# Performance work log

Measured on AMD Instinct MI355X. Metric: run time of the kernel, lower is better.

## Reference

```python
import jax, jax.numpy as jnp
import numpy as np

K = 256           # number of selected features (init kwarg k)
NUM_SAMPLES = 8   # init kwarg num_samples
BATCH = 256
NUM_FEATURES = 20000


def setup_inputs() -> dict:
    key = jax.random.key(0)
    logits = jax.random.normal(key, (BATCH, NUM_FEATURES, 1), dtype=jnp.float32)
    return {"logits": logits, "tau": 1, "training": 0}


def reference(logits, tau, training):
    # Eval branch of SubsetLayer.forward (training=False).
    # logits: [B, N, 1]
    B, N, _ = logits.shape
    scores = logits[..., 0]                       # [B, N]
    _, idx = jax.lax.top_k(scores, K)             # idx: [B, K]
    # k-hot mask built directly by scatter (equivalent to one_hot(...).sum(1))
    khot = jnp.zeros((B, N), dtype=jnp.float32)
    khot = khot.at[jnp.arange(B)[:, None], idx].set(1.0)  # [B, N]
    # unsqueeze(0).unsqueeze(-1).expand(num_samples, -1, -1, -1)
    out = jnp.broadcast_to(khot[None, :, :, None], (NUM_SAMPLES, B, N, 1))
    return out
```

## Files before the change

kernel.cpp:

```cpp
#include <hip/hip_runtime.h>

#define BATCH   256
#define NFEAT   20000
#define NVEC    (NFEAT / 4)
#define KSEL    256
#define NSAMP   8
#define CAP     2048

typedef unsigned long long u64;
typedef float __attribute__((ext_vector_type(4))) f32x4;

__device__ __forceinline__ unsigned fmap(float f) {
    unsigned u = __float_as_uint(f);
    return (u & 0x80000000u) ? ~u : (u | 0x80000000u);
}

__device__ __forceinline__ void select_bin_wave0(const unsigned* hist, int nbins, int w,
                                                 int* s_d, int* s_w, int lane) {
    for (int base = nbins - 1; base >= 0; base -= 64) {
        int bin = base - lane;
        unsigned c = (bin >= 0) ? hist[bin] : 0u;
        unsigned p = c;
#pragma unroll
        for (int off = 1; off < 64; off <<= 1) {
            unsigned t = __shfl_up(p, off);
            if (lane >= off) p += t;
        }
        unsigned long long m = __ballot(p >= (unsigned)w);
        if (m) {
            int l = __ffsll(m) - 1;
            if (lane == l) { *s_d = bin; *s_w = w - (int)(p - c); }
            return;
        }
        w -= (int)__shfl(p, 63);
    }
    if (lane == 0) { *s_d = 0; *s_w = 1; }
}

__device__ __forceinline__ void pick64(const unsigned* arr, int w, int lane,
                                       int* s_idx, int* s_w) {
    unsigned c = arr[63 - lane];
    unsigned p = c;
#pragma unroll
    for (int off = 1; off < 64; off <<= 1) {
        unsigned t = __shfl_up(p, off);
        if (lane >= off) p += t;
    }
    unsigned long long m = __ballot(p >= (unsigned)w);
    if (m) {
        int l = __ffsll(m) - 1;
        if (lane == l) { *s_idx = 63 - l; *s_w = w - (int)(p - c); }
    } else if (lane == 0) { *s_idx = 0; *s_w = 1; }
}

__global__ __launch_bounds__(1024) void topk_select(const float* __restrict__ logits,
                                                    u64* __restrict__ rowthr) {
    const int b = blockIdx.x, tid = threadIdx.x;
    const int lane = tid & 63, wave = tid >> 6;
    const float4* __restrict__ row4 = (const float4*)(logits + (size_t)b * NFEAT);

    __shared__ unsigned hist[4096];
    __shared__ u64 cand[CAP];
    __shared__ unsigned csum[64];
    __shared__ int s_d, s_w;
    __shared__ unsigned s_cnt;
    __shared__ u64 s_thr;
    __shared__ int s_run, s_cut, s_wc[16];

    float4 v[5];
#pragma unroll
    for (int j = 0; j < 5; ++j) {
        const int i4 = tid + j * 1024;
        v[j] = row4[(i4 < NVEC) ? i4 : (NVEC - 1)];
    }
#pragma unroll
    for (int j = 0; j < 4; ++j) hist[tid + j * 1024] = 0;
    __syncthreads();

    unsigned kk[5][4];
#pragma unroll
    for (int j = 0; j < 5; ++j) {
        kk[j][0] = fmap(v[j].x); kk[j][1] = fmap(v[j].y);
        kk[j][2] = fmap(v[j].z); kk[j][3] = fmap(v[j].w);
    }
#pragma unroll
    for (int j = 0; j < 4; ++j) {
#pragma unroll
        for (int e = 0; e < 4; ++e) atomicAdd(&hist[kk[j][e] >> 20], 1u);
    }
    if (tid + 4096 < NVEC) {
#pragma unroll
        for (int e = 0; e < 4; ++e) atomicAdd(&hist[kk[4][e] >> 20], 1u);
    }
    __syncthreads();

    unsigned keypref; int w;
    {
#pragma unroll
        for (int j = 0; j < 4; ++j) {
            const int c = wave * 4 + j;
            unsigned x = hist[c * 64 + lane];
#pragma unroll
            for (int off = 32; off; off >>= 1) x += __shfl_down(x, off);
            if (lane == 0) csum[c] = x;
        }
        __syncthreads();
        if (wave == 0) pick64(csum, KSEL, lane, &s_d, &s_w);
        __syncthreads();
        const int chunk = s_d; const int w0 = s_w;
        if (wave == 0) pick64(&hist[chunk * 64], w0, lane, &s_d, &s_w);
        if (tid == 0) s_cnt = 0;
        __syncthreads();
        keypref = (unsigned)(chunk * 64 + s_d);
        w = s_w;
    }
    int shift = 20;

    unsigned C;
    for (;;) {
#pragma unroll
        for (int j = 0; j < 5; ++j) {
            const int i4 = tid + j * 1024;
            if (i4 < NVEC) {
#pragma unroll
                for (int e = 0; e < 4; ++e) {
                    const unsigned k = kk[j][e];
                    if ((k >> shift) == keypref) {
                        unsigned p = atomicAdd(&s_cnt, 1u);
                        if (p < CAP) cand[p] = ((u64)k << 32) | (unsigned)~(4 * i4 + e);
                    }
                }
            }
        }
        __syncthreads();
        C = s_cnt;
        if (C <= CAP || shift == 0) break;

        const int nb = (shift >= 12) ? 12 : shift;
        const int nsh = shift - nb;
        for (int i = tid; i < (1 << nb); i += 1024) hist[i] = 0;
        __syncthreads();
#pragma unroll
        for (int j = 0; j < 5; ++j) {
            const int i4 = tid + j * 1024;
            if (i4 < NVEC) {
#pragma unroll
                for (int e = 0; e < 4; ++e) {
                    const unsigned k = kk[j][e];
                    if ((k >> shift) == keypref)
                        atomicAdd(&hist[(k >> nsh) & ((1u << nb) - 1u)], 1u);
                }
            }
        }
        __syncthreads();
        if (wave == 0) select_bin_wave0(hist, 1 << nb, w, &s_d, &s_w, lane);
        if (tid == 0) s_cnt = 0;
        __syncthreads();
        keypref = (keypref << nb) | (unsigned)s_d;
        w = s_w;
        shift = nsh;
    }

    if (C <= CAP) {
        for (int i = tid; i < (int)C; i += 1024) {
            const u64 ci = cand[i];
            int cgt = 0;
            for (int j = 0; j < (int)C; ++j) cgt += (cand[j] > ci) ? 1 : 0;
            if (cgt == w - 1) s_thr = ci;
        }
        __syncthreads();
    } else {
        if (tid == 0) { s_run = 0; s_cut = 0; }
        __syncthreads();
#pragma unroll 1
        for (int j = 0; j < 5; ++j) {
            const int i4 = tid + j * 1024;
            bool eq[4];
            int cnt4 = 0;
#pragma unroll
            for (int e = 0; e < 4; ++e) {
                eq[e] = (i4 < NVEC) && (kk[j][e] == keypref);
                cnt4 += eq[e] ? 1 : 0;
            }
            unsigned p = (unsigned)cnt4;
#pragma unroll
            for (int off = 1; off < 64; off <<= 1) {
                unsigned t = __shfl_up(p, off);
                if (lane >= off) p += t;
            }
            const unsigned excl = p - (unsigned)cnt4;
            if (lane == 63) s_wc[wave] = (int)p;
            __syncthreads();
            int off0 = s_run + (int)excl;
            for (int x = 0; x < wave; ++x) off0 += s_wc[x];
#pragma unroll
            for (int e = 0; e < 4; ++e) {
                if (eq[e]) { if (off0 == w - 1) s_cut = 4 * i4 + e; ++off0; }
            }
            __syncthreads();
            if (tid == 0) { int t = 0; for (int x = 0; x < 16; ++x) t += s_wc[x]; s_run += t; }
            __syncthreads();
            if (s_run >= w) break;
        }
        if (tid == 0) s_thr = ((u64)keypref << 32) | (unsigned)~s_cut;
        __syncthreads();
    }

    if (tid == 0) rowthr[b] = s_thr;
}

__global__ __launch_bounds__(256) void write_out(const float* __restrict__ logits,
                                                 const u64* __restrict__ rowthr,
                                                 float* __restrict__ out) {
    const int b = blockIdx.y;
    const int q = blockIdx.x * 256 + threadIdx.x;
    if (q >= NVEC) return;

    const u64 thr = rowthr[b];
    const unsigned thr_k = (unsigned)(thr >> 32);
    const unsigned thr_l = (unsigned)thr;
    const int n = q * 4;
    const float4 v = *reinterpret_cast<const float4*>(logits + (size_t)b * NFEAT + n);

    f32x4 m;
    {
        const float* vf = &v.x;
#pragma unroll
        for (int j = 0; j < 4; ++j) {
            const unsigned k = fmap(vf[j]);
            const bool sel = (k > thr_k) || (k == thr_k && (unsigned)~(n + j) >= thr_l);
            m[j] = sel ? 1.0f : 0.0f;
        }
    }

#pragma unroll
    for (int s = 0; s < NSAMP; ++s) {
        *reinterpret_cast<f32x4*>(out + ((size_t)s * BATCH + b) * NFEAT + n) = m;
    }
}

extern "C" void kernel_launch(void* const* d_in, const int* in_sizes, int n_in,
                              void* d_out, int out_size, void* d_ws, size_t ws_size,
                              hipStream_t stream) {
    const float* logits = (const float*)d_in[0];
    float* out = (float*)d_out;
    u64* rowthr = (u64*)d_ws;

    topk_select<<<BATCH, 1024, 0, stream>>>(logits, rowthr);

    dim3 grid((NVEC + 255) / 256, BATCH);
    write_out<<<grid, 256, 0, stream>>>(logits, rowthr, out);
}
```

Before: 41.38 us.

## Replace candidate-buffer rank sort with iterative 8-bit radix refinement until unique

The top-k threshold search no longer collects candidates into a shared buffer and ranks them with an O(C^2) pairwise count. It keeps refining the key prefix with 8-bit histogram passes, each using a two-level pick64 scan, until the selected bin holds a single element or all bits are resolved. This removes the quadratic candidate ranking and the 16KB candidate array from shared memory. In exchange it may need several more histogram passes and barriers per row.

```diff
diff --git a/kernel.cpp b/kernel.cpp
--- a/kernel.cpp
+++ b/kernel.cpp
@@ -5,7 +5,6 @@
 #define NVEC    (NFEAT / 4)
 #define KSEL    256
 #define NSAMP   8
-#define CAP     2048
 
 typedef unsigned long long u64;
 typedef float __attribute__((ext_vector_type(4))) f32x4;
@@ -13,28 +12,6 @@
 __device__ __forceinline__ unsigned fmap(float f) {
     unsigned u = __float_as_uint(f);
     return (u & 0x80000000u) ? ~u : (u | 0x80000000u);
-}
-
-__device__ __forceinline__ void select_bin_wave0(const unsigned* hist, int nbins, int w,
-                                                 int* s_d, int* s_w, int lane) {
-    for (int base = nbins - 1; base >= 0; base -= 64) {
-        int bin = base - lane;
-        unsigned c = (bin >= 0) ? hist[bin] : 0u;
-        unsigned p = c;
-#pragma unroll
-        for (int off = 1; off < 64; off <<= 1) {
-            unsigned t = __shfl_up(p, off);
-            if (lane >= off) p += t;
-        }
-        unsigned long long m = __ballot(p >= (unsigned)w);
-        if (m) {
-            int l = __ffsll(m) - 1;
-            if (lane == l) { *s_d = bin; *s_w = w - (int)(p - c); }
-            return;
-        }
-        w -= (int)__shfl(p, 63);
-    }
-    if (lane == 0) { *s_d = 0; *s_w = 1; }
 }
 
 __device__ __forceinline__ void pick64(const unsigned* arr, int w, int lane,
@@ -60,10 +37,8 @@
     const float4* __restrict__ row4 = (const float4*)(logits + (size_t)b * NFEAT);
 
     __shared__ unsigned hist[4096];
-    __shared__ u64 cand[CAP];
     __shared__ unsigned csum[64];
     __shared__ int s_d, s_w;
-    __shared__ unsigned s_cnt;
     __shared__ u64 s_thr;
     __shared__ int s_run, s_cut, s_wc[16];
 
@@ -94,30 +69,38 @@
     }
     __syncthreads();
 
-    unsigned keypref; int w;
+    unsigned P; int w;
     {
 #pragma unroll
         for (int j = 0; j < 4; ++j) {
-            const int c = wave * 4 + j;
-            unsigned x = hist[c * 64 + lane];
+            const int cc = wave * 4 + j;
+            unsigned x = hist[cc * 64 + lane];
 #pragma unroll
             for (int off = 32; off; off >>= 1) x += __shfl_down(x, off);
-            if (lane == 0) csum[c] = x;
+            if (lane == 0) csum[cc] = x;
         }
         __syncthreads();
         if (wave == 0) pick64(csum, KSEL, lane, &s_d, &s_w);
         __syncthreads();
         const int chunk = s_d; const int w0 = s_w;
         if (wave == 0) pick64(&hist[chunk * 64], w0, lane, &s_d, &s_w);
-        if (tid == 0) s_cnt = 0;
-        __syncthreads();
-        keypref = (unsigned)(chunk * 64 + s_d);
+        __syncthreads();
+        P = (unsigned)(chunk * 64 + s_d);
         w = s_w;
     }
+    unsigned cnt = hist[P];
     int shift = 20;
 
-    unsigned C;
-    for (;;) {
+    while (cnt > 1u && shift > 0) {
+        const int nb  = (shift >= 8) ? 8 : shift;
+        const int nsh = shift - nb;
+        const int NB  = 1 << nb;
+        const int nz  = (NB > 64) ? NB : 64;
+        __syncthreads();
+        if (tid < nz) hist[tid] = 0;
+        if (tid >= 4 && tid < 64) csum[tid] = 0;
+        __syncthreads();
+
 #pragma unroll
         for (int j = 0; j < 5; ++j) {
             const int i4 = tid + j * 1024;
@@ -125,21 +108,40 @@
 #pragma unroll
                 for (int e = 0; e < 4; ++e) {
                     const unsigned k = kk[j][e];
-                    if ((k >> shift) == keypref) {
-                        unsigned p = atomicAdd(&s_cnt, 1u);
-                        if (p < CAP) cand[p] = ((u64)k << 32) | (unsigned)~(4 * i4 + e);
-                    }
+                    if ((k >> shift) == P)
+                        atomicAdd(&hist[(k >> nsh) & (unsigned)(NB - 1)], 1u);
                 }
             }
         }
         __syncthreads();
-        C = s_cnt;
-        if (C <= CAP || shift == 0) break;
-
-        const int nb = (shift >= 12) ? 12 : shift;
-        const int nsh = shift - nb;
-        for (int i = tid; i < (1 << nb); i += 1024) hist[i] = 0;
-        __syncthreads();
+
+        unsigned d;
+        if (NB > 64) {
+            if (wave < 4) {
+                unsigned x = hist[wave * 64 + lane];
+#pragma unroll
+                for (int off = 32; off; off >>= 1) x += __shfl_down(x, off);
+                if (lane == 0) csum[wave] = x;
+            }
+            __syncthreads();
+            if (wave == 0) pick64(csum, w, lane, &s_d, &s_w);
+            __syncthreads();
+            const int chunk2 = s_d; const int w1 = s_w;
+            if (wave == 0) pick64(&hist[chunk2 * 64], w1, lane, &s_d, &s_w);
+            __syncthreads();
+            d = (unsigned)(chunk2 * 64 + s_d);
+        } else {
+            if (wave == 0) pick64(hist, w, lane, &s_d, &s_w);
+            __syncthreads();
+            d = (unsigned)s_d;
+        }
+        w = s_w;
+        cnt = hist[d];
+        P = (P << nb) | d;
+        shift = nsh;
+    }
+
+    if (cnt == 1u) {
 #pragma unroll
         for (int j = 0; j < 5; ++j) {
             const int i4 = tid + j * 1024;
@@ -147,26 +149,10 @@
 #pragma unroll
                 for (int e = 0; e < 4; ++e) {
                     const unsigned k = kk[j][e];
-                    if ((k >> shift) == keypref)
-                        atomicAdd(&hist[(k >> nsh) & ((1u << nb) - 1u)], 1u);
+                    if ((k >> shift) == P)
+                        s_thr = ((u64)k << 32) | (unsigned)~(4 * i4 + e);
                 }
             }
-        }
-        __syncthreads();
-        if (wave == 0) select_bin_wave0(hist, 1 << nb, w, &s_d, &s_w, lane);
-        if (tid == 0) s_cnt = 0;
-        __syncthreads();
-        keypref = (keypref << nb) | (unsigned)s_d;
-        w = s_w;
-        shift = nsh;
-    }
-
-    if (C <= CAP) {
-        for (int i = tid; i < (int)C; i += 1024) {
-            const u64 ci = cand[i];
-            int cgt = 0;
-            for (int j = 0; j < (int)C; ++j) cgt += (cand[j] > ci) ? 1 : 0;
-            if (cgt == w - 1) s_thr = ci;
         }
         __syncthreads();
     } else {
@@ -179,7 +165,7 @@
             int cnt4 = 0;
 #pragma unroll
             for (int e = 0; e < 4; ++e) {
-                eq[e] = (i4 < NVEC) && (kk[j][e] == keypref);
+                eq[e] = (i4 < NVEC) && (kk[j][e] == P);
                 cnt4 += eq[e] ? 1 : 0;
             }
             unsigned p = (unsigned)cnt4;
@@ -202,7 +188,7 @@
             __syncthreads();
             if (s_run >= w) break;
         }
-        if (tid == 0) s_thr = ((u64)keypref << 32) | (unsigned)~s_cut;
+        if (tid == 0) s_thr = ((u64)P << 32) | (unsigned)~s_cut;
         __syncthreads();
     }
 
```

Result: no change. 41.81 us (+1.0%).
